# Performance work log

Hardware: AMD Instinct MI355X
Metric: run time of the kernel (lower is better)

## Reference

```python
import jax, jax.numpy as jnp
import numpy as np

B, C, H, W = 4, 256, 64, 64
CQK = C // 8  # query/key projection dim = 32


def setup_inputs() -> dict:
    key = jax.random.key(0)
    ks = jax.random.split(key, 9)
    inp = {
        "input": jax.random.normal(ks[0], (B, C, H, W), dtype=jnp.float32),
        "structure": jax.random.normal(ks[1], (B, C, H, W), dtype=jnp.float32),
        "style": jax.random.normal(ks[2], (B, C, H, W), dtype=jnp.float32),
        # 1x1 conv weights stored as [out, in] (kernel spatial dims are 1)
        "Wq": jax.random.normal(ks[3], (CQK, C), dtype=jnp.float32) * (1.0 / np.sqrt(C)),
        "bq": jax.random.normal(ks[4], (CQK,), dtype=jnp.float32) * 0.01,
        "Wk": jax.random.normal(ks[5], (CQK, C), dtype=jnp.float32) * (1.0 / np.sqrt(C)),
        "bk": jax.random.normal(ks[6], (CQK,), dtype=jnp.float32) * 0.01,
        "Wv": jax.random.normal(ks[7], (C, C), dtype=jnp.float32) * (1.0 / np.sqrt(C)),
        "bv": jax.random.normal(ks[8], (C,), dtype=jnp.float32) * 0.01,
    }
    return inp


def reference(input, structure, style, Wq, bq, Wk, bk, Wv, bv):
    b, c, h, w = input.shape
    n = h * w
    # 1x1 convs == per-pixel channel GEMMs
    q = jnp.einsum('bchw,oc->bohw', input, Wq) + bq[None, :, None, None]
    k = jnp.einsum('bchw,oc->bohw', structure, Wk) + bk[None, :, None, None]
    v = jnp.einsum('bchw,oc->bohw', style, Wv) + bv[None, :, None, None]
    q = q.reshape(b, -1, n).transpose(0, 2, 1)   # [B, N, CQK]
    k = k.reshape(b, -1, n)                      # [B, CQK, N]
    v = v.reshape(b, -1, n)                      # [B, C, N]
    scores = jnp.einsum('bnc,bcm->bnm', q, k)    # [B, N, N], no 1/sqrt(d) scaling (as in source)
    # source subtracts the GLOBAL max of the score tensor (scalar), then softmax(dim=-1)
    attn = jax.nn.softmax(scores - jnp.max(scores), axis=-1)
    # out = value @ attn^T : out[b,c,i] = sum_j v[b,c,j] * attn[b,i,j]
    out = jnp.einsum('bcj,bij->bci', v, attn)
    return out.reshape(b, c, h, w)
```

## Files before the change

kernel.cpp:

```cpp
#include <hip/hip_runtime.h>
#include <hip/hip_bf16.h>
#include <math.h>

typedef __attribute__((ext_vector_type(8))) short short8;
typedef __attribute__((ext_vector_type(4))) short short4v;
typedef __attribute__((ext_vector_type(4))) float f32x4;

#define LOG2E 1.44269504088896f

__device__ __forceinline__ unsigned short f2bf(float f) {
  union { float f; unsigned int u; } v; v.f = f;
  unsigned int r = v.u + 0x7fffu + ((v.u >> 16) & 1u);
  return (unsigned short)(r >> 16);
}
__device__ __forceinline__ float bf2f(unsigned short h) {
  union { unsigned int u; float f; } v; v.u = ((unsigned int)h) << 16;
  return v.f;
}

__global__ void k_wtrans(const float* __restrict__ Wq, const float* __restrict__ Wk,
                         float* __restrict__ wt) {
  for (int i = threadIdx.x; i < 32 * 256; i += 256) {
    int d = i >> 8, c = i & 255;
    wt[c * 64 + d] = Wq[i];
    wt[c * 64 + 32 + d] = Wk[i];
  }
}

__global__ __launch_bounds__(256) void k_qkproj(
    const float* __restrict__ input, const float* __restrict__ structure,
    const float* __restrict__ wt, const float* __restrict__ bq, const float* __restrict__ bk,
    unsigned short* __restrict__ qh, unsigned short* __restrict__ ql,
    unsigned short* __restrict__ kh) {
  __shared__ float red[2 * 64 * 65];
  const int b = blockIdx.y;
  const int n0 = blockIdx.x * 64;
  const int wu = __builtin_amdgcn_readfirstlane(threadIdx.x >> 6);
  const int l = threadIdx.x & 63;
  const size_t ibase = ((size_t)b << 20) + (size_t)(n0 + l);

  float aq[32], ak[32];
#pragma unroll
  for (int d = 0; d < 32; ++d) { aq[d] = 0.f; ak[d] = 0.f; }

#pragma unroll 2
  for (int cc = 0; cc < 64; ++cc) {
    const int c = wu * 64 + cc;
    const float xq = input[ibase + ((size_t)c << 12)];
    const float xk = structure[ibase + ((size_t)c << 12)];
    const float* wr = wt + c * 64;
#pragma unroll
    for (int d = 0; d < 32; ++d) {
      aq[d] = fmaf(wr[d], xq, aq[d]);
      ak[d] = fmaf(wr[32 + d], xk, ak[d]);
    }
  }
  float* myred = red + ((wu & 1) * 64 + l) * 65;
  if (wu < 2) {
#pragma unroll
    for (int d = 0; d < 32; ++d) { myred[d] = aq[d]; myred[32 + d] = ak[d]; }
  }
  __syncthreads();
  if (wu >= 2) {
#pragma unroll
    for (int d = 0; d < 32; ++d) { myred[d] += aq[d]; myred[32 + d] += ak[d]; }
  }
  __syncthreads();

  const int p = threadIdx.x & 63;
  const int half = (threadIdx.x >> 6) & 1;
  const int dh = threadIdx.x >> 7;
  const float* bias = half ? bk : bq;
  const float scl = half ? 1.0f : LOG2E;
  unsigned short hs[16], lo[16];
#pragma unroll
  for (int d2 = 0; d2 < 16; ++d2) {
    const int d = dh * 16 + d2;
    float v = red[p * 65 + half * 32 + d] + red[(64 + p) * 65 + half * 32 + d];
    v = (v + bias[d]) * scl;
    unsigned short h = f2bf(v);
    hs[d2] = h;
    lo[d2] = f2bf(v - bf2f(h));
  }
  const size_t row = ((size_t)b << 12) + (size_t)(n0 + p);
  if (!half) {
    unsigned short* dsth = qh + row * 32 + dh * 16;
    unsigned short* dstl = ql + row * 32 + dh * 16;
#pragma unroll
    for (int i2 = 0; i2 < 2; ++i2) {
      uint4 t, t2;
      t.x = (unsigned)hs[i2*8+0] | ((unsigned)hs[i2*8+1] << 16);
      t.y = (unsigned)hs[i2*8+2] | ((unsigned)hs[i2*8+3] << 16);
      t.z = (unsigned)hs[i2*8+4] | ((unsigned)hs[i2*8+5] << 16);
      t.w = (unsigned)hs[i2*8+6] | ((unsigned)hs[i2*8+7] << 16);
      t2.x = (unsigned)lo[i2*8+0] | ((unsigned)lo[i2*8+1] << 16);
      t2.y = (unsigned)lo[i2*8+2] | ((unsigned)lo[i2*8+3] << 16);
      t2.z = (unsigned)lo[i2*8+4] | ((unsigned)lo[i2*8+5] << 16);
      t2.w = (unsigned)lo[i2*8+6] | ((unsigned)lo[i2*8+7] << 16);
      ((uint4*)dsth)[i2] = t;
      ((uint4*)dstl)[i2] = t2;
    }
  } else {
    unsigned short* dsth = kh + row * 32 + dh * 16;
#pragma unroll
    for (int i2 = 0; i2 < 2; ++i2) {
      uint4 t;
      t.x = (unsigned)hs[i2*8+0] | ((unsigned)hs[i2*8+1] << 16);
      t.y = (unsigned)hs[i2*8+2] | ((unsigned)hs[i2*8+3] << 16);
      t.z = (unsigned)hs[i2*8+4] | ((unsigned)hs[i2*8+5] << 16);
      t.w = (unsigned)hs[i2*8+6] | ((unsigned)hs[i2*8+7] << 16);
      ((uint4*)dsth)[i2] = t;
    }
  }
}

__global__ __launch_bounds__(256) void k_caststyle(const float* __restrict__ style,
                                                   unsigned short* __restrict__ xsf) {
  const int b = blockIdx.z, ct = blockIdx.y;
  const int n = blockIdx.x * 256 + threadIdx.x;
  const float* src = style + ((size_t)b << 20) + (((size_t)(ct * 64)) << 12) + (size_t)n;
  const int ntile = n >> 4, m = n & 15;
#pragma unroll
  for (int gq = 0; gq < 8; ++gq) {
    uint4 t;
    unsigned vv[4];
#pragma unroll
    for (int q2 = 0; q2 < 4; ++q2) {
      unsigned short a = f2bf(src[((size_t)(gq * 8 + q2 * 2)) << 12]);
      unsigned short bb = f2bf(src[((size_t)(gq * 8 + q2 * 2 + 1)) << 12]);
      vv[q2] = (unsigned)a | ((unsigned)bb << 16);
    }
    t.x = vv[0]; t.y = vv[1]; t.z = vv[2]; t.w = vv[3];
    const int kc = ct * 2 + (gq >> 2);
    const int g = gq & 3;
    const size_t fa = ((((size_t)(b * 256 + ntile)) * 8 + kc) * 64 + g * 16 + m) * 8;
    *(uint4*)(xsf + fa) = t;
  }
}

__global__ __launch_bounds__(256) void k_vgemm(const unsigned short* __restrict__ xsf,
                                               const float* __restrict__ Wv,
                                               const float* __restrict__ bv,
                                               unsigned short* __restrict__ vws) {
  const int b = blockIdx.z, coT = blockIdx.y, nT = blockIdx.x;
  const int w = threadIdx.x >> 6, l = threadIdx.x & 63;
  const int m = l & 15, g = l >> 4;
  const int co0 = coT * 64 + w * 16;
  const int n0 = nT * 128;
  f32x4 acc[8];
#pragma unroll
  for (int f = 0; f < 8; ++f) { acc[f][0]=0.f; acc[f][1]=0.f; acc[f][2]=0.f; acc[f][3]=0.f; }

#pragma unroll 2
  for (int kc = 0; kc < 8; ++kc) {
    const int c0 = kc * 32 + g * 8;
    const float* wp = Wv + (size_t)(co0 + m) * 256 + c0;
    float4 a0 = *(const float4*)wp;
    float4 a1 = *(const float4*)(wp + 4);
    short8 af;
    af[0]=(short)f2bf(a0.x); af[1]=(short)f2bf(a0.y); af[2]=(short)f2bf(a0.z); af[3]=(short)f2bf(a0.w);
    af[4]=(short)f2bf(a1.x); af[5]=(short)f2bf(a1.y); af[6]=(short)f2bf(a1.z); af[7]=(short)f2bf(a1.w);
#pragma unroll
    for (int f = 0; f < 8; ++f) {
      const short8 bfr = *(const short8*)(xsf +
        ((((size_t)(b * 256 + (nT * 8 + f))) * 8 + kc) * 64 + l) * 8);
      acc[f] = __builtin_amdgcn_mfma_f32_16x16x32_bf16(af, bfr, acc[f], 0, 0, 0);
    }
  }
  float4 bvv = *(const float4*)(bv + co0 + g * 4);
  const float bvr[4] = {bvv.x, bvv.y, bvv.z, bvv.w};
#pragma unroll
  for (int f = 0; f < 8; ++f)
#pragma unroll
    for (int r = 0; r < 4; ++r) {
      const int co = co0 + g * 4 + r;
      const int n = n0 + f * 16 + m;
      vws[(((size_t)(b * 256 + co)) << 12) + n] = f2bf(acc[f][r] + bvr[r]);
    }
}

#define P_PANEL  16384
#define P_BUF    32768
#define LDS_TOT  65536

__global__ __launch_bounds__(512, 2) void k_flash(
    const unsigned short* __restrict__ qh_ws, const unsigned short* __restrict__ ql_ws,
    const unsigned short* __restrict__ kh_ws, const unsigned short* __restrict__ v_ws,
    float* __restrict__ out0, unsigned short* __restrict__ pacc1,
    float* __restrict__ pl) {
  __shared__ char lds[LDS_TOT];
  const int bid = blockIdx.x;
  const int qt = bid >> 3;
  const int b = (bid >> 1) & 3;
  const int jh = bid & 1;
  const int tid = threadIdx.x;
  const int w = __builtin_amdgcn_readfirstlane(tid >> 6);
  const int l = tid & 63;
  const int m = l & 15, g = l >> 4;

  const size_t qrow = (((size_t)b << 12) + (size_t)(qt * 128 + w * 16 + m)) * 32 + g * 8;
  const short8 qhf = *(const short8*)(qh_ws + qrow);
  const short8 qlf = *(const short8*)(ql_ws + qrow);

  f32x4 acc[8][2];
#pragma unroll
  for (int it = 0; it < 8; ++it)
#pragma unroll
    for (int ct = 0; ct < 2; ++ct) { acc[it][ct][0]=0.f; acc[it][ct][1]=0.f; acc[it][ct][2]=0.f; acc[it][ct][3]=0.f; }
  float lsum[4];
#pragma unroll
  for (int r = 0; r < 4; ++r) lsum[r] = 0.f;

  const int jbase = jh * 2048;
  for (int jt = 0; jt < 16; ++jt) {
    const int j128 = jbase + jt * 128;
    const int pb = jt & 1;
    char* Pb = lds + pb * P_BUF;
    short8 vbf[4][2];
#pragma unroll
    for (int ks = 0; ks < 4; ++ks)
#pragma unroll
      for (int ct = 0; ct < 2; ++ct)
        vbf[ks][ct] = *(const short8*)(v_ws +
          (((size_t)(b * 256 + w * 32 + ct * 16 + m)) << 12) + j128 + ks * 32 + g * 8);
    short8 khv[8];
#pragma unroll
    for (int t = 0; t < 8; ++t)
      khv[t] = *(const short8*)(kh_ws + (((size_t)b << 12) + (size_t)(j128 + t * 16 + m)) * 32 + g * 8);
    f32x4 sv[8];
#pragma unroll
    for (int t = 0; t < 8; ++t) {
      f32x4 z = {0.f, 0.f, 0.f, 0.f};
      f32x4 s0 = __builtin_amdgcn_mfma_f32_16x16x32_bf16(qhf, khv[t], z, 0, 0, 0);
      sv[t] = __builtin_amdgcn_mfma_f32_16x16x32_bf16(qlf, khv[t], s0, 0, 0, 0);
    }
#pragma unroll
    for (int t = 0; t < 8; ++t)
#pragma unroll
      for (int r = 0; r < 4; ++r) {
        const float p = exp2f(sv[t][r]);
        lsum[r] += p;
        const int row = w * 16 + g * 4 + r;
        const int cw2 = (t & 3) * 32 + 2 * m;
        *(unsigned short*)(Pb + (t >> 2) * P_PANEL + row * 128 + (cw2 ^ ((row & 7) << 4))) = f2bf(p);
      }
    __syncthreads();
#pragma unroll
    for (int ks = 0; ks < 4; ++ks) {
      short8 pa[8];
#pragma unroll
      for (int it = 0; it < 8; ++it) {
        const int row = it * 16 + m;
        pa[it] = *(const short8*)(Pb + (ks >> 1) * P_PANEL + row * 128 +
                                  (((ks & 1) * 64 + g * 16) ^ ((row & 7) << 4)));
      }
#pragma unroll
      for (int ct = 0; ct < 2; ++ct)
#pragma unroll
        for (int it = 0; it < 8; ++it)
          acc[it][ct] = __builtin_amdgcn_mfma_f32_16x16x32_bf16(pa[it], vbf[ks][ct], acc[it][ct], 0, 0, 0);
    }
  }
#pragma unroll
  for (int d = 1; d <= 8; d <<= 1)
#pragma unroll
    for (int r = 0; r < 4; ++r) lsum[r] += __shfl_xor(lsum[r], d);
  if (m == 0) {
#pragma unroll
    for (int r = 0; r < 4; ++r) {
      const int row = qt * 128 + w * 16 + g * 4 + r;
      pl[(size_t)jh * 16384 + ((size_t)b << 12) + row] = lsum[r];
    }
  }
  if (jh == 0) {
#pragma unroll
    for (int it = 0; it < 8; ++it)
#pragma unroll
      for (int ct = 0; ct < 2; ++ct) {
        const int c = w * 32 + ct * 16 + m;
        float4 o;
        o.x = acc[it][ct][0]; o.y = acc[it][ct][1]; o.z = acc[it][ct][2]; o.w = acc[it][ct][3];
        *(float4*)(out0 + (((size_t)(b * 256 + c)) << 12) + qt * 128 + it * 16 + g * 4) = o;
      }
  } else {
#pragma unroll
    for (int it = 0; it < 8; ++it)
#pragma unroll
      for (int ct = 0; ct < 2; ++ct) {
        const int c = w * 32 + ct * 16 + m;
        short4v o;
        o[0] = (short)f2bf(acc[it][ct][0]); o[1] = (short)f2bf(acc[it][ct][1]);
        o[2] = (short)f2bf(acc[it][ct][2]); o[3] = (short)f2bf(acc[it][ct][3]);
        *(short4v*)(pacc1 + (((size_t)(b * 256 + c)) << 12) + qt * 128 + it * 16 + g * 4) = o;
      }
  }
}

__global__ __launch_bounds__(256) void k_combine(float* o, const unsigned short* __restrict__ pacc1,
                                                 const float* __restrict__ pl) {
  const int b = blockIdx.y;
  const int n = blockIdx.x * 64 + (threadIdx.x & 63);
  const int c0 = (threadIdx.x >> 6) * 64;
  const size_t mi = ((size_t)b << 12) + n;
  const float rl = 1.0f / (pl[mi] + pl[16384 + mi]);
#pragma unroll 4
  for (int ci = 0; ci < 64; ++ci) {
    const size_t a = (((size_t)(b * 256 + c0 + ci)) << 12) + n;
    o[a] = (o[a] + bf2f(pacc1[a])) * rl;
  }
}

extern "C" void kernel_launch(void* const* d_in, const int* in_sizes, int n_in,
                              void* d_out, int out_size, void* d_ws, size_t ws_size,
                              hipStream_t stream) {
  (void)in_sizes; (void)n_in; (void)out_size; (void)ws_size;
  const float* input     = (const float*)d_in[0];
  const float* structure = (const float*)d_in[1];
  const float* style     = (const float*)d_in[2];
  const float* Wq = (const float*)d_in[3];
  const float* bq = (const float*)d_in[4];
  const float* Wk = (const float*)d_in[5];
  const float* bk = (const float*)d_in[6];
  const float* Wv = (const float*)d_in[7];
  const float* bv = (const float*)d_in[8];
  float* out = (float*)d_out;
  char* ws = (char*)d_ws;

  float* wt           = (float*)(ws);
  unsigned short* qh  = (unsigned short*)(ws + 65536);
  unsigned short* ql  = (unsigned short*)(ws + 65536 + 1048576);
  unsigned short* kh  = (unsigned short*)(ws + 65536 + 2097152);
  unsigned short* vw  = (unsigned short*)(ws + 65536 + 3145728);
  unsigned short* xsf = (unsigned short*)(ws + 65536 + 3145728 + 8388608);
  unsigned short* pacc1 = xsf;
  float* pl           = (float*)(ws + 20119552);

  k_wtrans<<<dim3(1), dim3(256), 0, stream>>>(Wq, Wk, wt);
  k_qkproj<<<dim3(64, 4), dim3(256), 0, stream>>>(input, structure, wt, bq, bk, qh, ql, kh);
  k_caststyle<<<dim3(16, 4, 4), dim3(256), 0, stream>>>(style, xsf);
  k_vgemm<<<dim3(32, 4, 4), dim3(256), 0, stream>>>(xsf, Wv, bv, vw);
  k_flash<<<dim3(256), dim3(512), 0, stream>>>(qh, ql, kh, vw, out, pacc1, pl);
  k_combine<<<dim3(64, 4), dim3(256), 0, stream>>>(out, pacc1, pl);
}
```

Measured before the change: 145.6 us.

## Split flash attention output channels across two blocks to double grid size

Measured after the change: 159.4 us. 1.1x slower.

```diff
diff --git a/kernel.cpp b/kernel.cpp
--- a/kernel.cpp
+++ b/kernel.cpp
@@ -183,16 +183,17 @@
 #define P_BUF    32768
 #define LDS_TOT  65536
 
-__global__ __launch_bounds__(512, 2) void k_flash(
+__global__ __launch_bounds__(512, 4) void k_flash(
     const unsigned short* __restrict__ qh_ws, const unsigned short* __restrict__ ql_ws,
     const unsigned short* __restrict__ kh_ws, const unsigned short* __restrict__ v_ws,
     float* __restrict__ out0, unsigned short* __restrict__ pacc1,
     float* __restrict__ pl) {
   __shared__ char lds[LDS_TOT];
   const int bid = blockIdx.x;
-  const int qt = bid >> 3;
-  const int b = (bid >> 1) & 3;
-  const int jh = bid & 1;
+  const int qt = bid >> 4;
+  const int b = (bid >> 2) & 3;
+  const int jh = (bid >> 1) & 1;
+  const int ch = bid & 1;
   const int tid = threadIdx.x;
   const int w = __builtin_amdgcn_readfirstlane(tid >> 6);
   const int l = tid & 63;
@@ -202,27 +203,24 @@
   const short8 qhf = *(const short8*)(qh_ws + qrow);
   const short8 qlf = *(const short8*)(ql_ws + qrow);
 
-  f32x4 acc[8][2];
-#pragma unroll
-  for (int it = 0; it < 8; ++it)
-#pragma unroll
-    for (int ct = 0; ct < 2; ++ct) { acc[it][ct][0]=0.f; acc[it][ct][1]=0.f; acc[it][ct][2]=0.f; acc[it][ct][3]=0.f; }
+  f32x4 acc[8];
+#pragma unroll
+  for (int it = 0; it < 8; ++it) { acc[it][0]=0.f; acc[it][1]=0.f; acc[it][2]=0.f; acc[it][3]=0.f; }
   float lsum[4];
 #pragma unroll
   for (int r = 0; r < 4; ++r) lsum[r] = 0.f;
 
+  const int cch = ch * 128 + w * 16 + m;
   const int jbase = jh * 2048;
   for (int jt = 0; jt < 16; ++jt) {
     const int j128 = jbase + jt * 128;
     const int pb = jt & 1;
     char* Pb = lds + pb * P_BUF;
-    short8 vbf[4][2];
+    short8 vbf[4];
 #pragma unroll
     for (int ks = 0; ks < 4; ++ks)
-#pragma unroll
-      for (int ct = 0; ct < 2; ++ct)
-        vbf[ks][ct] = *(const short8*)(v_ws +
-          (((size_t)(b * 256 + w * 32 + ct * 16 + m)) << 12) + j128 + ks * 32 + g * 8);
+      vbf[ks] = *(const short8*)(v_ws +
+        (((size_t)(b * 256 + cch)) << 12) + j128 + ks * 32 + g * 8);
     short8 khv[8];
 #pragma unroll
     for (int t = 0; t < 8; ++t)
@@ -255,17 +253,15 @@
                                   (((ks & 1) * 64 + g * 16) ^ ((row & 7) << 4)));
       }
 #pragma unroll
-      for (int ct = 0; ct < 2; ++ct)
-#pragma unroll
-        for (int it = 0; it < 8; ++it)
-          acc[it][ct] = __builtin_amdgcn_mfma_f32_16x16x32_bf16(pa[it], vbf[ks][ct], acc[it][ct], 0, 0, 0);
+      for (int it = 0; it < 8; ++it)
+        acc[it] = __builtin_amdgcn_mfma_f32_16x16x32_bf16(pa[it], vbf[ks], acc[it], 0, 0, 0);
     }
   }
 #pragma unroll
   for (int d = 1; d <= 8; d <<= 1)
 #pragma unroll
     for (int r = 0; r < 4; ++r) lsum[r] += __shfl_xor(lsum[r], d);
-  if (m == 0) {
+  if (m == 0 && ch == 0) {
 #pragma unroll
     for (int r = 0; r < 4; ++r) {
       const int row = qt * 128 + w * 16 + g * 4 + r;
@@ -274,25 +270,19 @@
   }
   if (jh == 0) {
 #pragma unroll
-    for (int it = 0; it < 8; ++it)
-#pragma unroll
-      for (int ct = 0; ct < 2; ++ct) {
-        const int c = w * 32 + ct * 16 + m;
-        float4 o;
-        o.x = acc[it][ct][0]; o.y = acc[it][ct][1]; o.z = acc[it][ct][2]; o.w = acc[it][ct][3];
-        *(float4*)(out0 + (((size_t)(b * 256 + c)) << 12) + qt * 128 + it * 16 + g * 4) = o;
-      }
+    for (int it = 0; it < 8; ++it) {
+      float4 o;
+      o.x = acc[it][0]; o.y = acc[it][1]; o.z = acc[it][2]; o.w = acc[it][3];
+      *(float4*)(out0 + (((size_t)(b * 256 + cch)) << 12) + qt * 128 + it * 16 + g * 4) = o;
+    }
   } else {
 #pragma unroll
-    for (int it = 0; it < 8; ++it)
-#pragma unroll
-      for (int ct = 0; ct < 2; ++ct) {
-        const int c = w * 32 + ct * 16 + m;
-        short4v o;
-        o[0] = (short)f2bf(acc[it][ct][0]); o[1] = (short)f2bf(acc[it][ct][1]);
-        o[2] = (short)f2bf(acc[it][ct][2]); o[3] = (short)f2bf(acc[it][ct][3]);
-        *(short4v*)(pacc1 + (((size_t)(b * 256 + c)) << 12) + qt * 128 + it * 16 + g * 4) = o;
-      }
+    for (int it = 0; it < 8; ++it) {
+      short4v o;
+      o[0] = (short)f2bf(acc[it][0]); o[1] = (short)f2bf(acc[it][1]);
+      o[2] = (short)f2bf(acc[it][2]); o[3] = (short)f2bf(acc[it][3]);
+      *(short4v*)(pacc1 + (((size_t)(b * 256 + cch)) << 12) + qt * 128 + it * 16 + g * 4) = o;
+    }
   }
 }
 
@@ -339,6 +329,6 @@
   k_qkproj<<<dim3(64, 4), dim3(256), 0, stream>>>(input, structure, wt, bq, bk, qh, ql, kh);
   k_caststyle<<<dim3(16, 4, 4), dim3(256), 0, stream>>>(style, xsf);
   k_vgemm<<<dim3(32, 4, 4), dim3(256), 0, stream>>>(xsf, Wv, bv, vw);
-  k_flash<<<dim3(256), dim3(512), 0, stream>>>(qh, ql, kh, vw, out, pacc1, pl);
+  k_flash<<<dim3(512), dim3(512), 0, stream>>>(qh, ql, kh, vw, out, pacc1, pl);
   k_combine<<<dim3(64, 4), dim3(256), 0, stream>>>(out, pacc1, pl);
 }
```
